# Optimization experiments

Measured on AMD Instinct MI355X. Metric: run time of the kernel, lower is better.

## Reference

```python
import jax, jax.numpy as jnp
import numpy as np

N = 100000
E = 1600000
D_IN = 50
D_H = 128
D_OUT = 128
EPS = 1e-5


def setup_inputs() -> dict:
    key = jax.random.key(0)
    ks = jax.random.split(key, 24)
    def w(k, shape, fan_in):
        return jax.random.normal(k, shape, jnp.float32) / np.sqrt(fan_in)
    inp = {
        'x': jax.random.normal(ks[0], (N, D_IN), jnp.float32),
        'edge_src': jax.random.randint(ks[1], (E,), 0, N, jnp.int32),
        'edge_dst': jax.random.randint(ks[2], (E,), 0, N, jnp.int32),
        # SAGEConv 1: D_IN -> D_H
        'Wl1': w(ks[3], (D_IN, D_H), D_IN), 'Wr1': w(ks[4], (D_IN, D_H), D_IN), 'b1': jnp.zeros((D_H,), jnp.float32),
        # SAGEConv 2: D_H -> D_H
        'Wl2': w(ks[5], (D_H, D_H), D_H), 'Wr2': w(ks[6], (D_H, D_H), D_H), 'b2': jnp.zeros((D_H,), jnp.float32),
        # SAGEConv 3: D_H -> D_OUT
        'Wl3': w(ks[7], (D_H, D_OUT), D_H), 'Wr3': w(ks[8], (D_H, D_OUT), D_H), 'b3': jnp.zeros((D_OUT,), jnp.float32),
        # skip linears (no bias)
        'Ws1': w(ks[9], (D_IN, D_H), D_IN), 'Ws2': w(ks[10], (D_IN, D_H), D_IN),
        # LayerNorm affine
        'lnw1': jnp.ones((D_H,), jnp.float32), 'lnb1': jnp.zeros((D_H,), jnp.float32),
        'lnw2': jnp.ones((D_H,), jnp.float32), 'lnb2': jnp.zeros((D_H,), jnp.float32),
        'lnw3': jnp.ones((D_OUT,), jnp.float32), 'lnb3': jnp.zeros((D_OUT,), jnp.float32),
        # PReLU scalar slopes (PyG init 0.25)
        'a1': jnp.float32(0.25), 'a2': jnp.float32(0.25), 'a3': jnp.float32(0.25),
    }
    return inp


def _sage(x, src, dst, Wl, Wr, b):
    # mean aggregation of source features at destinations, then linear + root
    msg = x[src]                                              # [E, d]
    agg = jax.ops.segment_sum(msg, dst, num_segments=N)       # [N, d]
    cnt = jax.ops.segment_sum(jnp.ones((src.shape[0],), x.dtype), dst, num_segments=N)
    mean = agg / jnp.maximum(cnt, 1.0)[:, None]
    return mean @ Wl + x @ Wr + b


def _graph_ln(x, w, b):
    # PyG LayerNorm mode='graph', batch=None: normalize over all nodes+channels
    xc = x - jnp.mean(x)
    std = jnp.sqrt(jnp.mean(xc * xc))
    return (xc / (std + EPS)) * w + b


def _prelu(x, a):
    return jnp.where(x >= 0, x, a * x)


def reference(x, edge_src, edge_dst, Wl1, Wr1, b1, Wl2, Wr2, b2, Wl3, Wr3, b3,
              Ws1, Ws2, lnw1, lnb1, lnw2, lnb2, lnw3, lnb3, a1, a2, a3):
    h1 = _sage(x, edge_src, edge_dst, Wl1, Wr1, b1)
    h1 = _prelu(_graph_ln(h1, lnw1, lnb1), a1)
    h2 = _sage(h1 + x @ Ws1, edge_src, edge_dst, Wl2, Wr2, b2)
    h2 = _prelu(_graph_ln(h2, lnw2, lnb2), a2)
    ret = _sage(h1 + h2 + x @ Ws2, edge_src, edge_dst, Wl3, Wr3, b3)
    ret = _prelu(_graph_ln(ret, lnw3, lnb3), a3)
    return ret
```

## Files before the change

### kernel.cpp

```cpp
#include <hip/hip_runtime.h>

#define D_IN 50
#define LN_EPS 1e-5f
#define BSH 8
#define MAXB 512

typedef __bf16 bf16_t;
typedef bf16_t bf16x8 __attribute__((ext_vector_type(8)));
typedef bf16_t bf16x4 __attribute__((ext_vector_type(4)));
typedef bf16_t bf16x2 __attribute__((ext_vector_type(2)));
typedef float f32x4_t __attribute__((ext_vector_type(4)));

#define ACC8(r, L, H)                                                        \
    {                                                                        \
        L[0] += __uint_as_float((r).x << 16);                                \
        H[0] += __uint_as_float((r).x & 0xffff0000u);                        \
        L[1] += __uint_as_float((r).y << 16);                                \
        H[1] += __uint_as_float((r).y & 0xffff0000u);                        \
        L[2] += __uint_as_float((r).z << 16);                                \
        H[2] += __uint_as_float((r).z & 0xffff0000u);                        \
        L[3] += __uint_as_float((r).w << 16);                                \
        H[3] += __uint_as_float((r).w & 0xffff0000u);                        \
    }

__global__ void bucket_hist_k(const int* __restrict__ dst, int* __restrict__ bcnt,
                              int e, int nb) {
    __shared__ int lh[MAXB];
    int t = threadIdx.x;
    for (int i = t; i < nb; i += 256) lh[i] = 0;
    __syncthreads();
    for (int i = blockIdx.x * 256 + t; i < e; i += gridDim.x * 256)
        atomicAdd(&lh[dst[i] >> BSH], 1);
    __syncthreads();
    for (int i = t; i < nb; i += 256) {
        int c = lh[i];
        if (c) atomicAdd(&bcnt[i * 16], c);
    }
}

__global__ void bscan_k(const int* __restrict__ bcnt, int* __restrict__ boff,
                        int* __restrict__ bpos, int nb, int e) {
    __shared__ int l[MAXB];
    int t = threadIdx.x;
    l[t] = (t < nb) ? bcnt[t * 16] : 0;
    __syncthreads();
    for (int off = 1; off < MAXB; off <<= 1) {
        int v = (t >= off) ? l[t - off] : 0;
        __syncthreads();
        l[t] += v;
        __syncthreads();
    }
    int excl = (t > 0) ? l[t - 1] : 0;
    if (t < nb) { boff[t] = excl; bpos[t * 16] = excl; }
    if (t == 0) boff[nb] = e;
}

__global__ void scatter_k(const int* __restrict__ src, const int* __restrict__ dst,
                          int* __restrict__ bpos, unsigned* __restrict__ pool,
                          int e, int nb) {
    __shared__ int lh[MAXB];
    __shared__ int lcur[MAXB];
    int t = threadIdx.x;
    for (int i = t; i < nb; i += 256) lh[i] = 0;
    __syncthreads();
    int chunk = (e + gridDim.x - 1) / gridDim.x;
    int s = blockIdx.x * chunk;
    int en = min(e, s + chunk);
    for (int i = s + t; i < en; i += 256)
        atomicAdd(&lh[dst[i] >> BSH], 1);
    __syncthreads();
    for (int i = t; i < nb; i += 256) {
        int c = lh[i];
        lcur[i] = c ? atomicAdd(&bpos[i * 16], c) : 0;
    }
    __syncthreads();
    for (int i = s + t; i < en; i += 256) {
        int d = dst[i];
        int p = atomicAdd(&lcur[d >> BSH], 1);
        pool[p] = (unsigned)src[i] | ((unsigned)(d & 255) << 17);
    }
}

__global__ void nhist_k(const unsigned* __restrict__ pool, const int* __restrict__ boff,
                        int* __restrict__ cnt, int n) {
    __shared__ int lc[256];
    int b = blockIdx.x, t = threadIdx.x;
    lc[t] = 0;
    __syncthreads();
    int s = boff[b], e = boff[b + 1];
    for (int i = s + t; i < e; i += 256) atomicAdd(&lc[pool[i] >> 17], 1);
    __syncthreads();
    int nd = (b << BSH) + t;
    if (nd < n) cnt[nd] = lc[t];
}

__global__ void scan_partial_k(const int* __restrict__ cnt, int* __restrict__ part, int n) {
    __shared__ int lds[256];
    int base = blockIdx.x * 1024;
    int t = threadIdx.x;
    int s = 0;
    for (int j = 0; j < 4; j++) {
        int idx = base + t * 4 + j;
        if (idx < n) s += cnt[idx];
    }
    lds[t] = s;
    __syncthreads();
    for (int off = 128; off > 0; off >>= 1) {
        if (t < off) lds[t] += lds[t + off];
        __syncthreads();
    }
    if (t == 0) part[blockIdx.x] = lds[0];
}

__global__ void scan_root_k(int* part, int nb) {
    __shared__ int l[256];
    int t = threadIdx.x;
    int v = (t < nb) ? part[t] : 0;
    l[t] = v;
    __syncthreads();
    for (int off = 1; off < 256; off <<= 1) {
        int x = (t >= off) ? l[t - off] : 0;
        __syncthreads();
        l[t] += x;
        __syncthreads();
    }
    if (t < nb) part[t] = l[t] - v;
}

__global__ void scan_final_k(const int* __restrict__ cnt, const int* __restrict__ part,
                             int* __restrict__ row_ptr, int n) {
    __shared__ int lds[256];
    int base = blockIdx.x * 1024;
    int t = threadIdx.x;
    int v[4];
    int s = 0;
    for (int j = 0; j < 4; j++) {
        int idx = base + t * 4 + j;
        v[j] = (idx < n) ? cnt[idx] : 0;
        s += v[j];
    }
    lds[t] = s;
    __syncthreads();
    for (int off = 1; off < 256; off <<= 1) {
        int xv = (t >= off) ? lds[t - off] : 0;
        __syncthreads();
        lds[t] += xv;
        __syncthreads();
    }
    int ex = (t > 0 ? lds[t - 1] : 0) + part[blockIdx.x];
    for (int j = 0; j < 4; j++) {
        int idx = base + t * 4 + j;
        if (idx < n) {
            row_ptr[idx] = ex;
            if (idx == n - 1) row_ptr[n] = ex + v[j];
            ex += v[j];
        }
    }
}

__global__ void cfill_k(const unsigned* __restrict__ pool, const int* __restrict__ boff,
                        const int* __restrict__ rp, int* __restrict__ col, int n) {
    __shared__ int lpos[256];
    int b = blockIdx.x, t = threadIdx.x;
    int nd = (b << BSH) + t;
    lpos[t] = (nd < n) ? rp[nd] : 0;
    __syncthreads();
    int s = boff[b], e = boff[b + 1];
    for (int i = s + t; i < e; i += 256) {
        unsigned pk = pool[i];
        int slot = atomicAdd(&lpos[pk >> 17], 1);
        col[slot] = (int)(pk & 0x1FFFFu);
    }
}

struct ConvDesc { const float* w; bf16_t* o; int kin; int kpad; };
struct ConvArgs { ConvDesc d[8]; };

__global__ void conv_w_k(ConvArgs args) {
    ConvDesc d = args.d[blockIdx.y];
    int i = blockIdx.x * 256 + threadIdx.x;
    int tot = 128 * d.kpad;
    if (i >= tot) return;
    int n = i / d.kpad, k = i - n * d.kpad;
    float v = (k < d.kin) ? d.w[(size_t)k * 128 + n] : 0.f;
    d.o[i] = (bf16_t)v;
}

__global__ void conv_x_k(const float* __restrict__ x, bf16_t* __restrict__ xb, int n) {
    int i = blockIdx.x * 256 + threadIdx.x;
    if (i >= n * 64) return;
    int node = i >> 6, k = i & 63;
    xb[i] = (k < D_IN) ? (bf16_t)x[node * D_IN + k] : (bf16_t)0.f;
}

__global__ void agg_bf64_k(const bf16_t* __restrict__ feat, const int* __restrict__ rp,
                           const int* __restrict__ col, bf16_t* __restrict__ mean, int n) {
    int wid = (blockIdx.x * blockDim.x + threadIdx.x) >> 6;
    int lane = threadIdx.x & 63;
    if (wid >= n) return;
    int start = rp[wid], end = rp[wid + 1];
    int lc = lane & 7;
    int g = lane >> 3;
    float aL[4], aH[4], bL[4], bH[4];
#pragma unroll
    for (int k = 0; k < 4; k++) { aL[k] = aH[k] = bL[k] = bH[k] = 0.f; }
    int e = start + g;
    for (; e + 8 < end; e += 16) {
        uint4 r0 = *(const uint4*)(feat + (size_t)col[e] * 64 + lc * 8);
        uint4 r1 = *(const uint4*)(feat + (size_t)col[e + 8] * 64 + lc * 8);
        ACC8(r0, aL, aH);
        ACC8(r1, bL, bH);
    }
    for (; e < end; e += 8) {
        uint4 r0 = *(const uint4*)(feat + (size_t)col[e] * 64 + lc * 8);
        ACC8(r0, aL, aH);
    }
#pragma unroll
    for (int k = 0; k < 4; k++) { aL[k] += bL[k]; aH[k] += bH[k]; }
#pragma unroll
    for (int off = 8; off < 64; off <<= 1) {
#pragma unroll
        for (int k = 0; k < 4; k++) {
            aL[k] += __shfl_xor(aL[k], off);
            aH[k] += __shfl_xor(aH[k], off);
        }
    }
    int c = end - start;
    float invc = 1.f / (float)(c > 0 ? c : 1);
    if (lane < 8) {
        bf16x8 o;
#pragma unroll
        for (int k = 0; k < 4; k++) {
            o[2 * k] = (bf16_t)(aL[k] * invc);
            o[2 * k + 1] = (bf16_t)(aH[k] * invc);
        }
        *(bf16x8*)(mean + (size_t)wid * 64 + lc * 8) = o;
    }
}

__global__ void agg_bf128_k(const bf16_t* __restrict__ feat, const int* __restrict__ rp,
                            const int* __restrict__ col, bf16_t* __restrict__ mean, int n) {
    int wid = (blockIdx.x * blockDim.x + threadIdx.x) >> 6;
    int lane = threadIdx.x & 63;
    if (wid >= n) return;
    int start = rp[wid], end = rp[wid + 1];
    int lc = lane & 15;
    int g = lane >> 4;
    float aL[4], aH[4], bL[4], bH[4];
#pragma unroll
    for (int k = 0; k < 4; k++) { aL[k] = aH[k] = bL[k] = bH[k] = 0.f; }
    int e = start + g;
    for (; e + 4 < end; e += 8) {
        uint4 r0 = *(const uint4*)(feat + (size_t)col[e] * 128 + lc * 8);
        uint4 r1 = *(const uint4*)(feat + (size_t)col[e + 4] * 128 + lc * 8);
        ACC8(r0, aL, aH);
        ACC8(r1, bL, bH);
    }
    for (; e < end; e += 4) {
        uint4 r0 = *(const uint4*)(feat + (size_t)col[e] * 128 + lc * 8);
        ACC8(r0, aL, aH);
    }
#pragma unroll
    for (int k = 0; k < 4; k++) { aL[k] += bL[k]; aH[k] += bH[k]; }
#pragma unroll
    for (int off = 16; off < 64; off <<= 1) {
#pragma unroll
        for (int k = 0; k < 4; k++) {
            aL[k] += __shfl_xor(aL[k], off);
            aH[k] += __shfl_xor(aH[k], off);
        }
    }
    int c = end - start;
    float invc = 1.f / (float)(c > 0 ? c : 1);
    if (lane < 16) {
        bf16x8 o;
#pragma unroll
        for (int k = 0; k < 4; k++) {
            o[2 * k] = (bf16_t)(aL[k] * invc);
            o[2 * k + 1] = (bf16_t)(aH[k] * invc);
        }
        *(bf16x8*)(mean + (size_t)wid * 128 + lc * 8) = o;
    }
}

template <int KPAD, bool DUAL, bool ACC>
__global__ __launch_bounds__(256) void mfma_gemm_k(
    const bf16_t* __restrict__ A, const bf16_t* __restrict__ B,
    const bf16_t* __restrict__ WlT, const bf16_t* __restrict__ WrT,
    const float* __restrict__ bias,
    bf16_t* __restrict__ out, float2* __restrict__ partials, int M) {
    constexpr int KC = KPAD / 32;
    constexpr int WELE = 8 * KC * 64 * 8;
    __shared__ bf16_t lwl[WELE];
    __shared__ bf16_t lwr[DUAL ? WELE : 8];

    const int tid = threadIdx.x;
    for (int ch = tid; ch < 8 * KC * 64; ch += 256) {
        int nt = ch / (KC * 64);
        int rem = ch - nt * (KC * 64);
        int c = rem >> 6;
        int ln = rem & 63;
        int m = ln & 15, q = ln >> 4;
        size_t srcoff = (size_t)(nt * 16 + m) * KPAD + c * 32 + q * 8;
        *(bf16x8*)&lwl[ch * 8] = *(const bf16x8*)(WlT + srcoff);
        if (DUAL) *(bf16x8*)&lwr[ch * 8] = *(const bf16x8*)(WrT + srcoff);
    }
    __syncthreads();

    const int wid = blockIdx.x * 4 + (tid >> 6);
    const int lane = tid & 63;
    const int row0 = wid * 32;
    if (row0 >= M) return;
    const int m = lane & 15;
    const int q = lane >> 4;

    bf16x8 af[2][KC], bfr[DUAL ? 2 : 1][DUAL ? KC : 1];
#pragma unroll
    for (int s = 0; s < 2; s++) {
        const bf16_t* ar = A + (size_t)(row0 + s * 16 + m) * KPAD + q * 8;
#pragma unroll
        for (int c = 0; c < KC; c++) af[s][c] = *(const bf16x8*)(ar + c * 32);
        if (DUAL) {
            const bf16_t* br = B + (size_t)(row0 + s * 16 + m) * KPAD + q * 8;
#pragma unroll
            for (int c = 0; c < KC; c++) bfr[s][c] = *(const bf16x8*)(br + c * 32);
        }
    }

    float lsum = 0.f, lsum2 = 0.f;
#pragma unroll
    for (int nt = 0; nt < 8; nt++) {
        f32x4_t acc0 = {0.f, 0.f, 0.f, 0.f};
        f32x4_t acc1 = {0.f, 0.f, 0.f, 0.f};
#pragma unroll
        for (int c = 0; c < KC; c++) {
            bf16x8 w = *(const bf16x8*)&lwl[((nt * KC + c) * 64 + lane) * 8];
            acc0 = __builtin_amdgcn_mfma_f32_16x16x32_bf16(af[0][c], w, acc0, 0, 0, 0);
            acc1 = __builtin_amdgcn_mfma_f32_16x16x32_bf16(af[1][c], w, acc1, 0, 0, 0);
        }
        if (DUAL) {
#pragma unroll
            for (int c = 0; c < KC; c++) {
                bf16x8 w = *(const bf16x8*)&lwr[((nt * KC + c) * 64 + lane) * 8];
                acc0 = __builtin_amdgcn_mfma_f32_16x16x32_bf16(bfr[0][c], w, acc0, 0, 0, 0);
                acc1 = __builtin_amdgcn_mfma_f32_16x16x32_bf16(bfr[1][c], w, acc1, 0, 0, 0);
            }
        }
        float bv = bias ? bias[nt * 16 + m] : 0.f;
#pragma unroll
        for (int s = 0; s < 2; s++) {
            f32x4_t* ap = (s == 0) ? &acc0 : &acc1;
#pragma unroll
            for (int r = 0; r < 4; r++) {
                int row = row0 + s * 16 + q * 4 + r;
                if (row < M) {
                    float o = (*ap)[r] + bv;
                    out[(size_t)row * 128 + nt * 16 + m] = (bf16_t)o;
                    if (ACC) { lsum += o; lsum2 += o * o; }
                }
            }
        }
    }
    if (ACC) {
        for (int off = 32; off > 0; off >>= 1) {
            lsum += __shfl_down(lsum, off);
            lsum2 += __shfl_down(lsum2, off);
        }
        if (lane == 0) partials[wid] = make_float2(lsum, lsum2);
    }
}

__global__ __launch_bounds__(256) void mfma_gemm3_k(
    const bf16_t* __restrict__ A, const bf16_t* __restrict__ B,
    const bf16_t* __restrict__ WlT, const bf16_t* __restrict__ WrT,
    const bf16_t* __restrict__ Ws1T, const bf16_t* __restrict__ Ws2T,
    const float* __restrict__ bias,
    bf16_t* __restrict__ outP, bf16_t* __restrict__ outC1, bf16_t* __restrict__ outC2,
    float2* __restrict__ partials, int M) {
    constexpr int KC = 2;
    constexpr int WELE = 8 * KC * 64 * 8;
    __shared__ bf16_t lwl[WELE];
    __shared__ bf16_t lwr[WELE];
    __shared__ bf16_t ls1[WELE];
    __shared__ bf16_t ls2[WELE];

    const int tid = threadIdx.x;
    for (int ch = tid; ch < 8 * KC * 64; ch += 256) {
        int nt = ch / (KC * 64);
        int rem = ch - nt * (KC * 64);
        int c = rem >> 6;
        int ln = rem & 63;
        int m = ln & 15, q = ln >> 4;
        size_t srcoff = (size_t)(nt * 16 + m) * 64 + c * 32 + q * 8;
        *(bf16x8*)&lwl[ch * 8] = *(const bf16x8*)(WlT + srcoff);
        *(bf16x8*)&lwr[ch * 8] = *(const bf16x8*)(WrT + srcoff);
        *(bf16x8*)&ls1[ch * 8] = *(const bf16x8*)(Ws1T + srcoff);
        *(bf16x8*)&ls2[ch * 8] = *(const bf16x8*)(Ws2T + srcoff);
    }
    __syncthreads();

    const int wid = blockIdx.x * 4 + (tid >> 6);
    const int lane = tid & 63;
    const int row0 = wid * 32;
    if (row0 >= M) return;
    const int m = lane & 15;
    const int q = lane >> 4;

    bf16x8 af[2][KC], bfr[2][KC];
#pragma unroll
    for (int s = 0; s < 2; s++) {
        const bf16_t* ar = A + (size_t)(row0 + s * 16 + m) * 64 + q * 8;
        const bf16_t* br = B + (size_t)(row0 + s * 16 + m) * 64 + q * 8;
#pragma unroll
        for (int c = 0; c < KC; c++) {
            af[s][c] = *(const bf16x8*)(ar + c * 32);
            bfr[s][c] = *(const bf16x8*)(br + c * 32);
        }
    }

    float lsum = 0.f, lsum2 = 0.f;
#pragma unroll
    for (int nt = 0; nt < 8; nt++) {
        f32x4_t aP0 = {0.f, 0.f, 0.f, 0.f}, aP1 = {0.f, 0.f, 0.f, 0.f};
        f32x4_t a10 = {0.f, 0.f, 0.f, 0.f}, a11 = {0.f, 0.f, 0.f, 0.f};
        f32x4_t a20 = {0.f, 0.f, 0.f, 0.f}, a21 = {0.f, 0.f, 0.f, 0.f};
#pragma unroll
        for (int c = 0; c < KC; c++) {
            int wi = ((nt * KC + c) * 64 + lane) * 8;
            bf16x8 wl = *(const bf16x8*)&lwl[wi];
            bf16x8 wr = *(const bf16x8*)&lwr[wi];
            bf16x8 w1 = *(const bf16x8*)&ls1[wi];
            bf16x8 w2 = *(const bf16x8*)&ls2[wi];
            aP0 = __builtin_amdgcn_mfma_f32_16x16x32_bf16(af[0][c], wl, aP0, 0, 0, 0);
            aP1 = __builtin_amdgcn_mfma_f32_16x16x32_bf16(af[1][c], wl, aP1, 0, 0, 0);
            aP0 = __builtin_amdgcn_mfma_f32_16x16x32_bf16(bfr[0][c], wr, aP0, 0, 0, 0);
            aP1 = __builtin_amdgcn_mfma_f32_16x16x32_bf16(bfr[1][c], wr, aP1, 0, 0, 0);
            a10 = __builtin_amdgcn_mfma_f32_16x16x32_bf16(bfr[0][c], w1, a10, 0, 0, 0);
            a11 = __builtin_amdgcn_mfma_f32_16x16x32_bf16(bfr[1][c], w1, a11, 0, 0, 0);
            a20 = __builtin_amdgcn_mfma_f32_16x16x32_bf16(bfr[0][c], w2, a20, 0, 0, 0);
            a21 = __builtin_amdgcn_mfma_f32_16x16x32_bf16(bfr[1][c], w2, a21, 0, 0, 0);
        }
        float bv = bias[nt * 16 + m];
#pragma unroll
        for (int s = 0; s < 2; s++) {
            f32x4_t* pP = (s == 0) ? &aP0 : &aP1;
            f32x4_t* p1 = (s == 0) ? &a10 : &a11;
            f32x4_t* p2 = (s == 0) ? &a20 : &a21;
#pragma unroll
            for (int r = 0; r < 4; r++) {
                int row = row0 + s * 16 + q * 4 + r;
                if (row < M) {
                    float o = (*pP)[r] + bv;
                    size_t oi = (size_t)row * 128 + nt * 16 + m;
                    outP[oi] = (bf16_t)o;
                    outC1[oi] = (bf16_t)(*p1)[r];
                    outC2[oi] = (bf16_t)(*p2)[r];
                    lsum += o; lsum2 += o * o;
                }
            }
        }
    }
    for (int off = 32; off > 0; off >>= 1) {
        lsum += __shfl_down(lsum, off);
        lsum2 += __shfl_down(lsum2, off);
    }
    if (lane == 0) partials[wid] = make_float2(lsum, lsum2);
}

__global__ void reduce_partials_k(const float2* __restrict__ p, int n,
                                  double* __restrict__ outp) {
    __shared__ double s1[256], s2[256];
    int t = threadIdx.x;
    double a = 0.0, b = 0.0;
    for (int i = t; i < n; i += 256) { a += (double)p[i].x; b += (double)p[i].y; }
    s1[t] = a; s2[t] = b;
    __syncthreads();
    for (int off = 128; off > 0; off >>= 1) {
        if (t < off) { s1[t] += s1[t + off]; s2[t] += s2[t + off]; }
        __syncthreads();
    }
    if (t == 0) { outp[0] = s1[0]; outp[1] = s2[0]; }
}

template <int MODE>
__global__ void ln_prelu_k(const bf16_t* __restrict__ pre, const bf16_t* __restrict__ h1in,
                           const bf16_t* __restrict__ s,
                           const float* __restrict__ lnw, const float* __restrict__ lnb,
                           const float* __restrict__ a_ptr, const double* __restrict__ acc,
                           void* __restrict__ out0v, void* __restrict__ out1v, int total) {
    int i = blockIdx.x * blockDim.x + threadIdx.x;
    if (i * 4 >= total) return;
    double cinv = 1.0 / (double)total;
    double mm = acc[0] * cinv;
    double var = acc[1] * cinv - mm * mm;
    float stdv = (float)sqrt(var > 0.0 ? var : 0.0);
    float scale = 1.0f / (stdv + LN_EPS);
    float mf = (float)mm;
    float a = a_ptr[0];
    int c4 = i & 31;
    float4 w = ((const float4*)lnw)[c4];
    float4 b = ((const float4*)lnb)[c4];
    bf16x4 p4 = ((const bf16x4*)pre)[i];
    float4 h;
    h.x = ((float)p4.x - mf) * scale * w.x + b.x;
    h.y = ((float)p4.y - mf) * scale * w.y + b.y;
    h.z = ((float)p4.z - mf) * scale * w.z + b.z;
    h.w = ((float)p4.w - mf) * scale * w.w + b.w;
    h.x = h.x >= 0.f ? h.x : a * h.x;
    h.y = h.y >= 0.f ? h.y : a * h.y;
    h.z = h.z >= 0.f ? h.z : a * h.z;
    h.w = h.w >= 0.f ? h.w : a * h.w;
    if (MODE == 1) {
        bf16x4 hb;
        hb.x = (bf16_t)h.x; hb.y = (bf16_t)h.y; hb.z = (bf16_t)h.z; hb.w = (bf16_t)h.w;
        ((bf16x4*)out0v)[i] = hb;
        bf16x4 sv = ((const bf16x4*)s)[i];
        bf16x4 tb;
        tb.x = (bf16_t)(h.x + (float)sv.x); tb.y = (bf16_t)(h.y + (float)sv.y);
        tb.z = (bf16_t)(h.z + (float)sv.z); tb.w = (bf16_t)(h.w + (float)sv.w);
        ((bf16x4*)out1v)[i] = tb;
    } else if (MODE == 2) {
        bf16x4 hv = ((const bf16x4*)h1in)[i];
        bf16x4 sv = ((const bf16x4*)s)[i];
        bf16x4 tb;
        tb.x = (bf16_t)((float)hv.x + h.x + (float)sv.x);
        tb.y = (bf16_t)((float)hv.y + h.y + (float)sv.y);
        tb.z = (bf16_t)((float)hv.z + h.z + (float)sv.z);
        tb.w = (bf16_t)((float)hv.w + h.w + (float)sv.w);
        ((bf16x4*)out0v)[i] = tb;
    } else {
        ((float4*)out0v)[i] = h;
    }
}

extern "C" void kernel_launch(void* const* d_in, const int* in_sizes, int n_in,
                              void* d_out, int out_size, void* d_ws, size_t ws_size,
                              hipStream_t stream) {
    const float* x    = (const float*)d_in[0];
    const int*   esrc = (const int*)d_in[1];
    const int*   edst = (const int*)d_in[2];
    const float* Wl1  = (const float*)d_in[3];
    const float* Wr1  = (const float*)d_in[4];
    const float* b1   = (const float*)d_in[5];
    const float* Wl2  = (const float*)d_in[6];
    const float* Wr2  = (const float*)d_in[7];
    const float* b2   = (const float*)d_in[8];
    const float* Wl3  = (const float*)d_in[9];
    const float* Wr3  = (const float*)d_in[10];
    const float* b3   = (const float*)d_in[11];
    const float* Ws1  = (const float*)d_in[12];
    const float* Ws2  = (const float*)d_in[13];
    const float* lnw1 = (const float*)d_in[14];
    const float* lnb1 = (const float*)d_in[15];
    const float* lnw2 = (const float*)d_in[16];
    const float* lnb2 = (const float*)d_in[17];
    const float* lnw3 = (const float*)d_in[18];
    const float* lnb3 = (const float*)d_in[19];
    const float* a1   = (const float*)d_in[20];
    const float* a2   = (const float*)d_in[21];
    const float* a3   = (const float*)d_in[22];

    const int N = in_sizes[0] / D_IN;
    const int E = in_sizes[1];
    const int NB = (N + 255) >> BSH;

    char* ws = (char*)d_ws;
    size_t off = 0;
    auto alloc = [&](size_t bytes) -> void* {
        void* p = ws + off;
        off += (bytes + 255) & ~(size_t)255;
        return p;
    };
    bf16_t* xb   = (bf16_t*)alloc((size_t)N * 64 * 2);
    bf16_t* mean = (bf16_t*)alloc((size_t)N * 128 * 2);
    bf16_t* PRE  = (bf16_t*)alloc((size_t)N * 128 * 2);
    bf16_t* C1   = (bf16_t*)alloc((size_t)N * 128 * 2);
    bf16_t* C2   = (bf16_t*)alloc((size_t)N * 128 * 2);
    bf16_t* h1b  = (bf16_t*)alloc((size_t)N * 128 * 2);
    bf16_t* TB   = (bf16_t*)alloc((size_t)N * 128 * 2);
    bf16_t* WT   = (bf16_t*)alloc((size_t)(4 * 128 * 64 + 4 * 128 * 128) * 2);
    int* cnt  = (int*)alloc((size_t)N * 4);
    int* rp   = (int*)alloc((size_t)(N + 1) * 4);
    int* col  = (int*)alloc((size_t)E * 4);
    int* part = (int*)alloc(512);
    int* bcnt = (int*)alloc((size_t)MAXB * 16 * 4);
    int* boff = (int*)alloc((size_t)(MAXB + 1) * 4);
    int* bpos = (int*)alloc((size_t)MAXB * 16 * 4);
    unsigned* pool = (unsigned*)alloc((size_t)E * 4);
    double* lnacc = (double*)alloc(6 * 8);
    const int tiles = (N + 31) / 32;
    float2* partials = (float2*)alloc((size_t)tiles * 8);

    bf16_t* Wl1T = WT;
    bf16_t* Wr1T = Wl1T + 128 * 64;
    bf16_t* Ws1T = Wr1T + 128 * 64;
    bf16_t* Ws2T = Ws1T + 128 * 64;
    bf16_t* Wl2T = Ws2T + 128 * 64;
    bf16_t* Wr2T = Wl2T + 128 * 128;
    bf16_t* Wl3T = Wr2T + 128 * 128;
    bf16_t* Wr3T = Wl3T + 128 * 128;

    hipMemsetAsync(bcnt, 0, (size_t)MAXB * 16 * 4, stream);

    const int NBS_n = (N + 1023) / 1024;
    bucket_hist_k<<<256, 256, 0, stream>>>(edst, bcnt, E, NB);
    bscan_k<<<1, MAXB, 0, stream>>>(bcnt, boff, bpos, NB, E);
    scatter_k<<<256, 256, 0, stream>>>(esrc, edst, bpos, pool, E, NB);
    nhist_k<<<NB, 256, 0, stream>>>(pool, boff, cnt, N);
    scan_partial_k<<<NBS_n, 256, 0, stream>>>(cnt, part, N);
    scan_root_k<<<1, 256, 0, stream>>>(part, NBS_n);
    scan_final_k<<<NBS_n, 256, 0, stream>>>(cnt, part, rp, N);
    cfill_k<<<NB, 256, 0, stream>>>(pool, boff, rp, col, N);

    ConvArgs ca;
    ca.d[0] = {Wl1, Wl1T, 50, 64};
    ca.d[1] = {Wr1, Wr1T, 50, 64};
    ca.d[2] = {Ws1, Ws1T, 50, 64};
    ca.d[3] = {Ws2, Ws2T, 50, 64};
    ca.d[4] = {Wl2, Wl2T, 128, 128};
    ca.d[5] = {Wr2, Wr2T, 128, 128};
    ca.d[6] = {Wl3, Wl3T, 128, 128};
    ca.d[7] = {Wr3, Wr3T, 128, 128};
    conv_w_k<<<dim3(64, 8), 256, 0, stream>>>(ca);
    conv_x_k<<<(N * 64 + 255) / 256, 256, 0, stream>>>(x, xb, N);

    const int aggBlocks = ((N * 64) + 255) / 256;
    const int gemmBlocks = (tiles + 3) / 4;
    const int lnBlocks = (N * 128 / 4 + 255) / 256;
    const int total = N * 128;

    agg_bf64_k<<<aggBlocks, 256, 0, stream>>>(xb, rp, col, mean, N);
    mfma_gemm3_k<<<gemmBlocks, 256, 0, stream>>>(
        mean, xb, Wl1T, Wr1T, Ws1T, Ws2T, b1, PRE, C1, C2, partials, N);
    reduce_partials_k<<<1, 256, 0, stream>>>(partials, tiles, lnacc + 0);
    ln_prelu_k<1><<<lnBlocks, 256, 0, stream>>>(
        PRE, nullptr, C1, lnw1, lnb1, a1, lnacc + 0, h1b, TB, total);

    agg_bf128_k<<<aggBlocks, 256, 0, stream>>>(TB, rp, col, mean, N);
    mfma_gemm_k<128, true, true><<<gemmBlocks, 256, 0, stream>>>(
        mean, TB, Wl2T, Wr2T, b2, PRE, partials, N);
    reduce_partials_k<<<1, 256, 0, stream>>>(partials, tiles, lnacc + 2);
    ln_prelu_k<2><<<lnBlocks, 256, 0, stream>>>(
        PRE, h1b, C2, lnw2, lnb2, a2, lnacc + 2, TB, nullptr, total);

    agg_bf128_k<<<aggBlocks, 256, 0, stream>>>(TB, rp, col, mean, N);
    mfma_gemm_k<128, true, true><<<gemmBlocks, 256, 0, stream>>>(
        mean, TB, Wl3T, Wr3T, b3, PRE, partials, N);
    reduce_partials_k<<<1, 256, 0, stream>>>(partials, tiles, lnacc + 4);
    ln_prelu_k<3><<<lnBlocks, 256, 0, stream>>>(
        PRE, nullptr, nullptr, lnw3, lnb3, a3, lnacc + 4, d_out, nullptr, total);
}
```

Before: 552.9 us.

## Fuse CSR scan, weight/x conversion and LN stat reduction to cut launches

Computes the row pointers inside the per-bucket histogram kernel with a block-local scan offset by the bucket start, which replaces three separate scan kernels. Merges the weight and x bf16 conversions into one launch. Removes the single-block partials reduction by having every ln_prelu block redundantly reduce the ~3125 per-tile partials in fp32 before normalizing. This trades fewer launches and serial single-block kernels for redundant reduction work in every LN block and lower-precision (float instead of double) variance accumulation.

```diff
diff --git a/kernel.cpp b/kernel.cpp
--- a/kernel.cpp
+++ b/kernel.cpp
@@ -81,81 +81,29 @@
     }
 }
 
-__global__ void nhist_k(const unsigned* __restrict__ pool, const int* __restrict__ boff,
-                        int* __restrict__ cnt, int n) {
+__global__ void nhist_rp_k(const unsigned* __restrict__ pool, const int* __restrict__ boff,
+                           int* __restrict__ rp, int n) {
     __shared__ int lc[256];
+    __shared__ int ls[256];
     int b = blockIdx.x, t = threadIdx.x;
     lc[t] = 0;
     __syncthreads();
     int s = boff[b], e = boff[b + 1];
     for (int i = s + t; i < e; i += 256) atomicAdd(&lc[pool[i] >> 17], 1);
     __syncthreads();
+    int v = lc[t];
+    ls[t] = v;
+    __syncthreads();
+    for (int off = 1; off < 256; off <<= 1) {
+        int x = (t >= off) ? ls[t - off] : 0;
+        __syncthreads();
+        ls[t] += x;
+        __syncthreads();
+    }
+    int excl = ls[t] - v;
     int nd = (b << BSH) + t;
-    if (nd < n) cnt[nd] = lc[t];
-}
-
-__global__ void scan_partial_k(const int* __restrict__ cnt, int* __restrict__ part, int n) {
-    __shared__ int lds[256];
-    int base = blockIdx.x * 1024;
-    int t = threadIdx.x;
-    int s = 0;
-    for (int j = 0; j < 4; j++) {
-        int idx = base + t * 4 + j;
-        if (idx < n) s += cnt[idx];
-    }
-    lds[t] = s;
-    __syncthreads();
-    for (int off = 128; off > 0; off >>= 1) {
-        if (t < off) lds[t] += lds[t + off];
-        __syncthreads();
-    }
-    if (t == 0) part[blockIdx.x] = lds[0];
-}
-
-__global__ void scan_root_k(int* part, int nb) {
-    __shared__ int l[256];
-    int t = threadIdx.x;
-    int v = (t < nb) ? part[t] : 0;
-    l[t] = v;
-    __syncthreads();
-    for (int off = 1; off < 256; off <<= 1) {
-        int x = (t >= off) ? l[t - off] : 0;
-        __syncthreads();
-        l[t] += x;
-        __syncthreads();
-    }
-    if (t < nb) part[t] = l[t] - v;
-}
-
-__global__ void scan_final_k(const int* __restrict__ cnt, const int* __restrict__ part,
-                             int* __restrict__ row_ptr, int n) {
-    __shared__ int lds[256];
-    int base = blockIdx.x * 1024;
-    int t = threadIdx.x;
-    int v[4];
-    int s = 0;
-    for (int j = 0; j < 4; j++) {
-        int idx = base + t * 4 + j;
-        v[j] = (idx < n) ? cnt[idx] : 0;
-        s += v[j];
-    }
-    lds[t] = s;
-    __syncthreads();
-    for (int off = 1; off < 256; off <<= 1) {
-        int xv = (t >= off) ? lds[t - off] : 0;
-        __syncthreads();
-        lds[t] += xv;
-        __syncthreads();
-    }
-    int ex = (t > 0 ? lds[t - 1] : 0) + part[blockIdx.x];
-    for (int j = 0; j < 4; j++) {
-        int idx = base + t * 4 + j;
-        if (idx < n) {
-            row_ptr[idx] = ex;
-            if (idx == n - 1) row_ptr[n] = ex + v[j];
-            ex += v[j];
-        }
-    }
+    if (nd < n) rp[nd] = s + excl;
+    if (nd == n - 1) rp[n] = e;
 }
 
 __global__ void cfill_k(const unsigned* __restrict__ pool, const int* __restrict__ boff,
@@ -176,21 +124,26 @@
 struct ConvDesc { const float* w; bf16_t* o; int kin; int kpad; };
 struct ConvArgs { ConvDesc d[8]; };
 
-__global__ void conv_w_k(ConvArgs args) {
-    ConvDesc d = args.d[blockIdx.y];
-    int i = blockIdx.x * 256 + threadIdx.x;
-    int tot = 128 * d.kpad;
-    if (i >= tot) return;
-    int n = i / d.kpad, k = i - n * d.kpad;
-    float v = (k < d.kin) ? d.w[(size_t)k * 128 + n] : 0.f;
-    d.o[i] = (bf16_t)v;
-}
-
-__global__ void conv_x_k(const float* __restrict__ x, bf16_t* __restrict__ xb, int n) {
-    int i = blockIdx.x * 256 + threadIdx.x;
-    if (i >= n * 64) return;
-    int node = i >> 6, k = i & 63;
-    xb[i] = (k < D_IN) ? (bf16_t)x[node * D_IN + k] : (bf16_t)0.f;
+__global__ void conv_all_k(ConvArgs args, const float* __restrict__ x,
+                           bf16_t* __restrict__ xb, int n) {
+    if (blockIdx.y == 0) {
+        int i = blockIdx.x * 256 + threadIdx.x;
+        if (i < n * 64) {
+            int node = i >> 6, k = i & 63;
+            xb[i] = (k < D_IN) ? (bf16_t)x[node * D_IN + k] : (bf16_t)0.f;
+        }
+    } else {
+        int d_idx = blockIdx.x >> 6;
+        if (d_idx < 8) {
+            ConvDesc d = args.d[d_idx];
+            int i = (blockIdx.x & 63) * 256 + threadIdx.x;
+            int tot = 128 * d.kpad;
+            if (i < tot) {
+                int nn = i / d.kpad, k = i - nn * d.kpad;
+                d.o[i] = (bf16_t)((k < d.kin) ? d.w[(size_t)k * 128 + nn] : 0.f);
+            }
+        }
+    }
 }
 
 __global__ void agg_bf64_k(const bf16_t* __restrict__ feat, const int* __restrict__ rp,
@@ -467,35 +420,38 @@
     if (lane == 0) partials[wid] = make_float2(lsum, lsum2);
 }
 
-__global__ void reduce_partials_k(const float2* __restrict__ p, int n,
-                                  double* __restrict__ outp) {
-    __shared__ double s1[256], s2[256];
-    int t = threadIdx.x;
-    double a = 0.0, b = 0.0;
-    for (int i = t; i < n; i += 256) { a += (double)p[i].x; b += (double)p[i].y; }
-    s1[t] = a; s2[t] = b;
-    __syncthreads();
-    for (int off = 128; off > 0; off >>= 1) {
-        if (t < off) { s1[t] += s1[t + off]; s2[t] += s2[t + off]; }
-        __syncthreads();
-    }
-    if (t == 0) { outp[0] = s1[0]; outp[1] = s2[0]; }
-}
-
 template <int MODE>
 __global__ void ln_prelu_k(const bf16_t* __restrict__ pre, const bf16_t* __restrict__ h1in,
                            const bf16_t* __restrict__ s,
                            const float* __restrict__ lnw, const float* __restrict__ lnb,
-                           const float* __restrict__ a_ptr, const double* __restrict__ acc,
+                           const float* __restrict__ a_ptr,
+                           const float2* __restrict__ partials, int nparts,
                            void* __restrict__ out0v, void* __restrict__ out1v, int total) {
-    int i = blockIdx.x * blockDim.x + threadIdx.x;
+    __shared__ float w1[4], w2[4];
+    int tid = threadIdx.x;
+    float ps = 0.f, ps2 = 0.f;
+    for (int i = tid; i < nparts; i += 256) {
+        float2 p = partials[i];
+        ps += p.x;
+        ps2 += p.y;
+    }
+    for (int off = 32; off > 0; off >>= 1) {
+        ps += __shfl_down(ps, off);
+        ps2 += __shfl_down(ps2, off);
+    }
+    int wave = tid >> 6, lane = tid & 63;
+    if (lane == 0) { w1[wave] = ps; w2[wave] = ps2; }
+    __syncthreads();
+    float sum = w1[0] + w1[1] + w1[2] + w1[3];
+    float sum2 = w2[0] + w2[1] + w2[2] + w2[3];
+
+    int i = blockIdx.x * blockDim.x + tid;
     if (i * 4 >= total) return;
-    double cinv = 1.0 / (double)total;
-    double mm = acc[0] * cinv;
-    double var = acc[1] * cinv - mm * mm;
-    float stdv = (float)sqrt(var > 0.0 ? var : 0.0);
+    float cinv = 1.0f / (float)total;
+    float mf = sum * cinv;
+    float var = sum2 * cinv - mf * mf;
+    float stdv = sqrtf(var > 0.f ? var : 0.f);
     float scale = 1.0f / (stdv + LN_EPS);
-    float mf = (float)mm;
     float a = a_ptr[0];
     int c4 = i & 31;
     float4 w = ((const float4*)lnw)[c4];
@@ -579,15 +535,12 @@
     bf16_t* h1b  = (bf16_t*)alloc((size_t)N * 128 * 2);
     bf16_t* TB   = (bf16_t*)alloc((size_t)N * 128 * 2);
     bf16_t* WT   = (bf16_t*)alloc((size_t)(4 * 128 * 64 + 4 * 128 * 128) * 2);
-    int* cnt  = (int*)alloc((size_t)N * 4);
     int* rp   = (int*)alloc((size_t)(N + 1) * 4);
     int* col  = (int*)alloc((size_t)E * 4);
-    int* part = (int*)alloc(512);
     int* bcnt = (int*)alloc((size_t)MAXB * 16 * 4);
     int* boff = (int*)alloc((size_t)(MAXB + 1) * 4);
     int* bpos = (int*)alloc((size_t)MAXB * 16 * 4);
     unsigned* pool = (unsigned*)alloc((size_t)E * 4);
-    double* lnacc = (double*)alloc(6 * 8);
     const int tiles = (N + 31) / 32;
     float2* partials = (float2*)alloc((size_t)tiles * 8);
 
@@ -602,14 +555,10 @@
 
     hipMemsetAsync(bcnt, 0, (size_t)MAXB * 16 * 4, stream);
 
-    const int NBS_n = (N + 1023) / 1024;
     bucket_hist_k<<<256, 256, 0, stream>>>(edst, bcnt, E, NB);
     bscan_k<<<1, MAXB, 0, stream>>>(bcnt, boff, bpos, NB, E);
     scatter_k<<<256, 256, 0, stream>>>(esrc, edst, bpos, pool, E, NB);
-    nhist_k<<<NB, 256, 0, stream>>>(pool, boff, cnt, N);
-    scan_partial_k<<<NBS_n, 256, 0, stream>>>(cnt, part, N);
-    scan_root_k<<<1, 256, 0, stream>>>(part, NBS_n);
-    scan_final_k<<<NBS_n, 256, 0, stream>>>(cnt, part, rp, N);
+    nhist_rp_k<<<NB, 256, 0, stream>>>(pool, boff, rp, N);
     cfill_k<<<NB, 256, 0, stream>>>(pool, boff, rp, col, N);
 
     ConvArgs ca;
@@ -621,8 +570,9 @@
     ca.d[5] = {Wr2, Wr2T, 128, 128};
     ca.d[6] = {Wl3, Wl3T, 128, 128};
     ca.d[7] = {Wr3, Wr3T, 128, 128};
-    conv_w_k<<<dim3(64, 8), 256, 0, stream>>>(ca);
-    conv_x_k<<<(N * 64 + 255) / 256, 256, 0, stream>>>(x, xb, N);
+    int convx = (N * 64 + 255) / 256;
+    if (convx < 512) convx = 512;
+    conv_all_k<<<dim3(convx, 2), 256, 0, stream>>>(ca, x, xb, N);
 
     const int aggBlocks = ((N * 64) + 255) / 256;
     const int gemmBlocks = (tiles + 3) / 4;
@@ -632,21 +582,18 @@
     agg_bf64_k<<<aggBlocks, 256, 0, stream>>>(xb, rp, col, mean, N);
     mfma_gemm3_k<<<gemmBlocks, 256, 0, stream>>>(
         mean, xb, Wl1T, Wr1T, Ws1T, Ws2T, b1, PRE, C1, C2, partials, N);
-    reduce_partials_k<<<1, 256, 0, stream>>>(partials, tiles, lnacc + 0);
     ln_prelu_k<1><<<lnBlocks, 256, 0, stream>>>(
-        PRE, nullptr, C1, lnw1, lnb1, a1, lnacc + 0, h1b, TB, total);
+        PRE, nullptr, C1, lnw1, lnb1, a1, partials, tiles, h1b, TB, total);
 
     agg_bf128_k<<<aggBlocks, 256, 0, stream>>>(TB, rp, col, mean, N);
     mfma_gemm_k<128, true, true><<<gemmBlocks, 256, 0, stream>>>(
         mean, TB, Wl2T, Wr2T, b2, PRE, partials, N);
-    reduce_partials_k<<<1, 256, 0, stream>>>(partials, tiles, lnacc + 2);
     ln_prelu_k<2><<<lnBlocks, 256, 0, stream>>>(
-        PRE, h1b, C2, lnw2, lnb2, a2, lnacc + 2, TB, nullptr, total);
+        PRE, h1b, C2, lnw2, lnb2, a2, partials, tiles, TB, nullptr, total);
 
     agg_bf128_k<<<aggBlocks, 256, 0, stream>>>(TB, rp, col, mean, N);
     mfma_gemm_k<128, true, true><<<gemmBlocks, 256, 0, stream>>>(
         mean, TB, Wl3T, Wr3T, b3, PRE, partials, N);
-    reduce_partials_k<<<1, 256, 0, stream>>>(partials, tiles, lnacc + 4);
     ln_prelu_k<3><<<lnBlocks, 256, 0, stream>>>(
-        PRE, nullptr, nullptr, lnw3, lnb3, a3, lnacc + 4, d_out, nullptr, total);
-}
+        PRE, nullptr, nullptr, lnw3, lnb3, a3, partials, tiles, d_out, nullptr, total);
+}
```

Result: slower. 589.5 us (+6.6%).
